# Performance work log

Measured on AMD Instinct MI355X. Metric: run time of the kernel, lower is better.

Reference implementation:

```python
import jax, jax.numpy as jnp
import numpy as np

TOPK = 13
N_CLASSES = 80
EPS = 1e-9
IOU_EPS = 1e-7


def _make_anchors():
    # YOLOv8 640x640, strides 8/16/32 -> 8400 anchor points (pixel coords, cell centers)
    pts, strides = [], []
    for s in (8, 16, 32):
        n = 640 // s
        c = (np.arange(n, dtype=np.float32) + 0.5) * s
        xs, ys = np.meshgrid(c, c)
        pts.append(np.stack([xs.ravel(), ys.ravel()], -1))
        strides.append(np.full((n * n, 1), s, np.float32))
    return np.concatenate(pts).astype(np.float32), np.concatenate(strides)


def setup_inputs() -> dict:
    key = jax.random.key(0)
    k1, k2, k3, k4, k5 = jax.random.split(key, 5)
    B, G, C = 64, 32, N_CLASSES
    anc, strd = _make_anchors()
    A = anc.shape[0]  # 8400
    # positive l,t,r,b distances so decoded pred boxes are valid
    dist = jnp.abs(jax.random.normal(k1, (B, 4, A))) * 16.0 + 1.0
    cls = jax.random.normal(k2, (B, C, A))
    preds = jnp.concatenate([dist, cls], axis=1)  # (B, 4+C, A)
    x1y1 = jax.random.uniform(k3, (B, G, 2)) * 560.0
    wh = jax.random.uniform(k4, (B, G, 2)) * 64.0 + 8.0
    gt_bboxes = jnp.concatenate([x1y1, x1y1 + wh], axis=-1)  # (B, G, 4) xyxy
    gt_classes = jax.random.randint(k5, (B, G), 0, C)
    return {"preds": preds, "gt_bboxes": gt_bboxes, "gt_classes": gt_classes,
            "anchor_points": jnp.asarray(anc), "stride_tensor": jnp.asarray(strd)}


def _iou_xyxy(a, b):
    # a: (B,A,1,4), b: (B,1,G,4) -> (B,A,G)
    lt = jnp.maximum(a[..., :2], b[..., :2])
    rb = jnp.minimum(a[..., 2:], b[..., 2:])
    wh = jnp.clip(rb - lt, 0.0)
    inter = wh[..., 0] * wh[..., 1]
    area_a = (a[..., 2] - a[..., 0]) * (a[..., 3] - a[..., 1])
    area_b = (b[..., 2] - b[..., 0]) * (b[..., 3] - b[..., 1])
    return inter / (area_a + area_b - inter + IOU_EPS)


def _assign(preds, gt_bboxes, gt_classes, anchor_points, stride_tensor):
    B, G, _ = gt_bboxes.shape
    A = anchor_points.shape[0]
    dist = jnp.transpose(preds[:, :4, :], (0, 2, 1))       # (B,A,4) l,t,r,b
    pred_cls = jnp.transpose(preds[:, 4:, :], (0, 2, 1))    # (B,A,C)
    # dist2bbox (xyxy)
    pb = jnp.concatenate([anchor_points[None] - dist[..., :2],
                          anchor_points[None] + dist[..., 2:]], axis=-1)  # (B,A,4)
    ious = _iou_xyxy(pb[:, :, None, :], gt_bboxes[:, None, :, :])          # (B,A,G)
    probs = jax.nn.softmax(pred_cls, axis=-1)                              # (B,A,C)
    idx_cls = jnp.broadcast_to(gt_classes[:, None, :], (B, A, G))
    cls_score = jnp.take_along_axis(probs, idx_cls, axis=-1)               # (B,A,G)
    align = jnp.sqrt(jnp.maximum(ious, 1e-12)) * jnp.sqrt(jnp.maximum(cls_score, 1e-12))
    # top-k over anchors (dim=1) -> scatter boolean mask
    mt = jnp.transpose(align, (0, 2, 1))                                   # (B,G,A)
    _, idx = jax.lax.top_k(mt, TOPK)                                       # (B,G,TOPK)
    bi = jnp.arange(B)[:, None, None]
    gi = jnp.arange(G)[None, :, None]
    mask = jnp.zeros((B, G, A), bool).at[bi, gi, idx].set(True)
    mask = jnp.transpose(mask, (0, 2, 1))                                  # (B,A,G)
    # anchors inside gt boxes
    d = jnp.concatenate([anchor_points[None, :, None, :] - gt_bboxes[:, None, :, :2],
                         gt_bboxes[:, None, :, 2:] - anchor_points[None, :, None, :]], axis=-1)
    mask = mask & (jnp.min(d, axis=-1) > EPS)
    # anchors assigned to multiple gts keep the highest-IoU gt
    multi = mask.sum(-1) > 1                                               # (B,A)
    best = jnp.argmax(ious, axis=-1)[..., None] == jnp.arange(G)[None, None, :]
    mask = jnp.where(multi[..., None], best, mask)
    fg = mask.any(-1)                                                      # (B,A)
    tgt_idx = jnp.argmax(mask, axis=-1)                                    # (B,A)
    tb = jnp.take_along_axis(gt_bboxes, tgt_idx[..., None], axis=1) * fg[..., None].astype(gt_bboxes.dtype)
    tc = jnp.where(fg, jnp.take_along_axis(gt_classes, tgt_idx, axis=1), 0)
    ts = jnp.take_along_axis(align, tgt_idx[..., None], axis=2)[..., 0] * fg.astype(align.dtype)
    return tb, tc, ts, fg, fg.sum()


def reference(preds, gt_bboxes, gt_classes, anchor_points, stride_tensor):
    return _assign(preds, gt_bboxes, gt_classes, anchor_points, stride_tensor)
```

## Files before the change

kernel.cpp:

```cpp
#include <hip/hip_runtime.h>
#include <cfloat>
#include <cstdint>
#include <climits>

#define NB 64
#define NG 32
#define NC 80
#define NA 8400
#define KTOP 13
#define CHUNK 256
#define NCH 33
#define NCAND (NCH * KTOP)
#define GGRP 16

#define CE(ka, ia, kb, ib)                                            \
    {                                                                 \
        const bool sw = (ka < kb) || (ka == kb && ia > ib);           \
        const unsigned tk = sw ? kb : ka;                             \
        const int      ti = sw ? ib : ia;                             \
        kb = sw ? ka : kb;  ib = sw ? ia : ib;                        \
        ka = tk;            ia = ti;                                  \
    }

__device__ __forceinline__ int wave_max_pos(int m) {
    m = max(m, __builtin_amdgcn_update_dpp(0, m, 0x111, 0xF, 0xF, true));
    m = max(m, __builtin_amdgcn_update_dpp(0, m, 0x112, 0xF, 0xF, true));
    m = max(m, __builtin_amdgcn_update_dpp(0, m, 0x114, 0xF, 0xF, true));
    m = max(m, __builtin_amdgcn_update_dpp(0, m, 0x118, 0xF, 0xF, true));
    m = max(m, __builtin_amdgcn_update_dpp(0, m, 0x142, 0xF, 0xF, true));
    m = max(m, __builtin_amdgcn_update_dpp(0, m, 0x143, 0xF, 0xF, true));
    return __builtin_amdgcn_readlane(m, 63);
}

__global__ __launch_bounds__(256, 2) void fusedAB(
    const float* __restrict__ preds,
    const float* __restrict__ gt_bboxes,
    const int*   __restrict__ gt_classes,
    const float* __restrict__ anchor_points,
    float2*      __restrict__ aux_ws,
    unsigned*    __restrict__ inside32,
    int*         __restrict__ bestg,
    float*       __restrict__ candv,
    int*         __restrict__ candi,
    float*       __restrict__ out_sum)
{
    __shared__ float sx1[NG], sy1[NG], sx2[NG], sy2[NG], sarea[NG];
    __shared__ int   scls[NG];
    __shared__ __align__(16) float salign[GGRP][CHUNK];
    __shared__ __align__(16) float sdist[4][CHUNK];

    const int tid   = threadIdx.x;
    const int chunk = blockIdx.x;
    const int b     = blockIdx.y;
    const int abase = chunk * CHUNK;
    const int a0    = abase + tid;
    const bool live = (a0 < NA);

    if (tid < NG) {
        const float* gb = gt_bboxes + ((size_t)b * NG + tid) * 4;
        const float x1 = gb[0], y1 = gb[1], x2 = gb[2], y2 = gb[3];
        sx1[tid] = x1; sy1[tid] = y1; sx2[tid] = x2; sy2[tid] = y2;
        sarea[tid] = (x2 - x1) * (y2 - y1);
        scls[tid]  = gt_classes[b * NG + tid];
    }
    if (b == 0 && chunk == 0 && tid == 0) out_sum[0] = 0.0f;

    {
        const int p = tid >> 6, k = tid & 63;
        float4 v = make_float4(0.0f, 0.0f, 0.0f, 0.0f);
        if (abase + 4 * k < NA)
            v = *(const float4*)(preds + ((size_t)b * (4 + NC) + p) * NA + abase + 4 * k);
        *(float4*)&sdist[p][4 * k] = v;
    }
    __syncthreads();

    float ax = 0, ay = 0, x1 = 0, y1 = 0, x2 = 0, y2 = 0, area = 0;
    if (live) {
        const float2 ap = *(const float2*)(anchor_points + (size_t)a0 * 2);
        ax = ap.x; ay = ap.y;
        const float l  = sdist[0][tid];
        const float t  = sdist[1][tid];
        const float r  = sdist[2][tid];
        const float bo = sdist[3][tid];
        x1 = ax - l; y1 = ay - t; x2 = ax + r; y2 = ay + bo;
        area = (x2 - x1) * (y2 - y1);
    }

    const float* cb = preds + ((size_t)b * (4 + NC) + 4) * NA + a0;

    float cls[NC];
    if (live) {
#pragma unroll
        for (int c = 0; c < NC; ++c) cls[c] = cb[(size_t)c * NA];
    } else {
#pragma unroll
        for (int c = 0; c < NC; ++c) cls[c] = 0.0f;
    }
#pragma unroll
    for (int c = 0; c < NC; ++c) asm volatile("" : "+v"(cls[c]));

    float m0 = cls[0], m1 = cls[1], m2 = cls[2], m3 = cls[3];
#pragma unroll
    for (int c = 4; c < NC; c += 4) {
        m0 = fmaxf(m0, cls[c]);
        m1 = fmaxf(m1, cls[c + 1]);
        m2 = fmaxf(m2, cls[c + 2]);
        m3 = fmaxf(m3, cls[c + 3]);
    }
    const float mx = fmaxf(fmaxf(m0, m1), fmaxf(m2, m3));

    float d = 0.0f;
#pragma unroll
    for (int c = 0; c < NC; ++c) d += __expf(cls[c] - mx);
    const float rd = 1.0f / d;

    unsigned ins = 0u;
    int   bg = 0;
    float bi = -1.0f;

    const int lane = tid & 63;
    const int wid  = tid >> 6;

    for (int grp = 0; grp < 2; ++grp) {
        if (live) {
            float cvl[GGRP];
#pragma unroll
            for (int gg = 0; gg < GGRP; ++gg)
                cvl[gg] = cb[(size_t)scls[grp * GGRP + gg] * NA];
#pragma unroll
            for (int gg = 0; gg < GGRP; ++gg) {
                const int g = grp * GGRP + gg;
                const float bx1 = sx1[g], by1 = sy1[g], bx2 = sx2[g], by2 = sy2[g];
                const float sag = sarea[g];
                const float ltx = fmaxf(x1, bx1), lty = fmaxf(y1, by1);
                const float rbx = fminf(x2, bx2), rby = fminf(y2, by2);
                const float w = fmaxf(rbx - ltx, 0.0f), h = fmaxf(rby - lty, 0.0f);
                const float inter = w * h;
                const float iou = inter / (area + sag - inter + 1e-7f);
                if (iou > bi) { bi = iou; bg = g; }
                const float cv = __expf(cvl[gg] - mx) * rd;
                const float al = sqrtf(fmaxf(iou, 1e-12f)) * sqrtf(fmaxf(cv, 1e-12f));
                const float dmin = fminf(fminf(ax - bx1, ay - by1), fminf(bx2 - ax, by2 - ay));
                if (dmin > 1e-9f) ins |= (1u << g);
                salign[gg][tid] = al;
            }
        } else {
#pragma unroll
            for (int gg = 0; gg < GGRP; ++gg) salign[gg][tid] = 0.0f;
        }
        __syncthreads();

        {
            const int gg0 = wid * 4;
            const float4 qA = *(const float4*)&salign[gg0 + 0][lane * 4];
            const float4 qB = *(const float4*)&salign[gg0 + 1][lane * 4];
            const float4 qC = *(const float4*)&salign[gg0 + 2][lane * 4];
            const float4 qD = *(const float4*)&salign[gg0 + 3][lane * 4];
            unsigned A0 = __float_as_uint(qA.x), A1 = __float_as_uint(qA.y);
            unsigned A2 = __float_as_uint(qA.z), A3 = __float_as_uint(qA.w);
            unsigned B0 = __float_as_uint(qB.x), B1 = __float_as_uint(qB.y);
            unsigned B2 = __float_as_uint(qB.z), B3 = __float_as_uint(qB.w);
            unsigned C0 = __float_as_uint(qC.x), C1 = __float_as_uint(qC.y);
            unsigned C2 = __float_as_uint(qC.z), C3 = __float_as_uint(qC.w);
            unsigned D0 = __float_as_uint(qD.x), D1 = __float_as_uint(qD.y);
            unsigned D2 = __float_as_uint(qD.z), D3 = __float_as_uint(qD.w);
            int IA0 = abase + lane * 4, IA1 = IA0 + 1, IA2 = IA0 + 2, IA3 = IA0 + 3;
            int IB0 = IA0, IB1 = IA1, IB2 = IA2, IB3 = IA3;
            int IC0 = IA0, IC1 = IA1, IC2 = IA2, IC3 = IA3;
            int ID0 = IA0, ID1 = IA1, ID2 = IA2, ID3 = IA3;

            CE(A0, IA0, A2, IA2); CE(A1, IA1, A3, IA3);
            CE(A0, IA0, A1, IA1); CE(A2, IA2, A3, IA3);
            CE(A1, IA1, A2, IA2);
            CE(B0, IB0, B2, IB2); CE(B1, IB1, B3, IB3);
            CE(B0, IB0, B1, IB1); CE(B2, IB2, B3, IB3);
            CE(B1, IB1, B2, IB2);
            CE(C0, IC0, C2, IC2); CE(C1, IC1, C3, IC3);
            CE(C0, IC0, C1, IC1); CE(C2, IC2, C3, IC3);
            CE(C1, IC1, C2, IC2);
            CE(D0, ID0, D2, ID2); CE(D1, ID1, D3, ID3);
            CE(D0, ID0, D1, ID1); CE(D2, ID2, D3, ID3);
            CE(D1, ID1, D2, ID2);

            unsigned rvA = 0u, rvB = 0u, rvC = 0u, rvD = 0u;
            int      riA = 0x7FFFFFFF, riB = 0x7FFFFFFF, riC = 0x7FFFFFFF, riD = 0x7FFFFFFF;
#pragma unroll
            for (int r = 0; r < KTOP; ++r) {
                const unsigned mA = (unsigned)wave_max_pos((int)A0);
                const unsigned mB = (unsigned)wave_max_pos((int)B0);
                const unsigned mC = (unsigned)wave_max_pos((int)C0);
                const unsigned mD = (unsigned)wave_max_pos((int)D0);
                const unsigned long long blA = __ballot(A0 == mA);
                const unsigned long long blB = __ballot(B0 == mB);
                const unsigned long long blC = __ballot(C0 == mC);
                const unsigned long long blD = __ballot(D0 == mD);
                const int wA = __ffsll(blA) - 1;
                const int wB = __ffsll(blB) - 1;
                const int wC = __ffsll(blC) - 1;
                const int wD = __ffsll(blD) - 1;
                const int xA = __builtin_amdgcn_readlane(IA0, wA);
                const int xB = __builtin_amdgcn_readlane(IB0, wB);
                const int xC = __builtin_amdgcn_readlane(IC0, wC);
                const int xD = __builtin_amdgcn_readlane(ID0, wD);
                if (lane == wA) { A0 = A1; IA0 = IA1; A1 = A2; IA1 = IA2; A2 = A3; IA2 = IA3; A3 = 0u; }
                if (lane == wB) { B0 = B1; IB0 = IB1; B1 = B2; IB1 = IB2; B2 = B3; IB2 = IB3; B3 = 0u; }
                if (lane == wC) { C0 = C1; IC0 = IC1; C1 = C2; IC1 = IC2; C2 = C3; IC2 = IC3; C3 = 0u; }
                if (lane == wD) { D0 = D1; ID0 = ID1; D1 = D2; ID1 = ID2; D2 = D3; ID2 = ID3; D3 = 0u; }
                if (lane == r) {
                    rvA = mA; riA = xA; rvB = mB; riB = xB;
                    rvC = mC; riC = xC; rvD = mD; riD = xD;
                }
            }
            if (lane < KTOP) {
                const int gbase = b * NG + grp * GGRP + gg0;
                const size_t b0 = ((size_t)(gbase + 0) * NCH + chunk) * KTOP + lane;
                const size_t b1 = ((size_t)(gbase + 1) * NCH + chunk) * KTOP + lane;
                const size_t b2 = ((size_t)(gbase + 2) * NCH + chunk) * KTOP + lane;
                const size_t b3 = ((size_t)(gbase + 3) * NCH + chunk) * KTOP + lane;
                candv[b0] = __uint_as_float(rvA);  candi[b0] = riA;
                candv[b1] = __uint_as_float(rvB);  candi[b1] = riB;
                candv[b2] = __uint_as_float(rvC);  candi[b2] = riC;
                candv[b3] = __uint_as_float(rvD);  candi[b3] = riD;
            }
        }
        __syncthreads();
    }

    if (live) {
        const int i = b * NA + a0;
        aux_ws[i] = make_float2(mx, rd);
        inside32[i] = ins;
        bestg[i]    = bg;
    }
}

__global__ __launch_bounds__(256) void mergeTopK(
    const float* __restrict__ candv,
    const int*   __restrict__ candi,
    int*         __restrict__ topk13)
{
    const int tid  = threadIdx.x;
    const int lane = tid & 63;
    const int row  = blockIdx.x * 4 + (tid >> 6);
    const size_t base = (size_t)row * NCAND;

    float v0 = -FLT_MAX, v1 = -FLT_MAX, v2 = -FLT_MAX, v3 = -FLT_MAX,
          v4 = -FLT_MAX, v5 = -FLT_MAX, v6 = -FLT_MAX;
    int   d0 = 0x7FFFFFFF, d1 = 0x7FFFFFFF, d2 = 0x7FFFFFFF, d3 = 0x7FFFFFFF,
          d4 = 0x7FFFFFFF, d5 = 0x7FFFFFFF, d6 = 0x7FFFFFFF;

#pragma unroll
    for (int k = 0; k < 7; ++k) {
        const int j0 = lane + 64 * k;
        if (j0 < NCAND) {
            const float x  = candv[base + j0];
            const int   xi = candi[base + j0];
            int r = 0;
            r += (v0 > x) || (v0 == x && d0 < xi);
            r += (v1 > x) || (v1 == x && d1 < xi);
            r += (v2 > x) || (v2 == x && d2 < xi);
            r += (v3 > x) || (v3 == x && d3 < xi);
            r += (v4 > x) || (v4 == x && d4 < xi);
            r += (v5 > x) || (v5 == x && d5 < xi);
            r += (v6 > x) || (v6 == x && d6 < xi);
            v6 = (6 < r) ? v6 : ((6 == r) ? x : v5);  d6 = (6 < r) ? d6 : ((6 == r) ? xi : d5);
            v5 = (5 < r) ? v5 : ((5 == r) ? x : v4);  d5 = (5 < r) ? d5 : ((5 == r) ? xi : d4);
            v4 = (4 < r) ? v4 : ((4 == r) ? x : v3);  d4 = (4 < r) ? d4 : ((4 == r) ? xi : d3);
            v3 = (3 < r) ? v3 : ((3 == r) ? x : v2);  d3 = (3 < r) ? d3 : ((3 == r) ? xi : d2);
            v2 = (2 < r) ? v2 : ((2 == r) ? x : v1);  d2 = (2 < r) ? d2 : ((2 == r) ? xi : d1);
            v1 = (1 < r) ? v1 : ((1 == r) ? x : v0);  d1 = (1 < r) ? d1 : ((1 == r) ? xi : d0);
            v0 = (0 == r) ? x  : v0;                  d0 = (0 == r) ? xi : d0;
        }
    }

    int ri = 0x7FFFFFFF;
#pragma unroll
    for (int rnd = 0; rnd < KTOP; ++rnd) {
        const int hk = __float_as_int(v0);
        const int mk = wave_max_pos(hk);
        const int key2 = (hk == mk) ? (INT_MAX - d0) : -1;
        const int mk2  = wave_max_pos(key2);
        const int midx = INT_MAX - mk2;
        if (hk == mk && d0 == midx) {
            v0 = v1; d0 = d1; v1 = v2; d1 = d2; v2 = v3; d2 = d3;
            v3 = v4; d3 = d4; v4 = v5; d4 = d5; v5 = v6; d5 = d6;
            v6 = -FLT_MAX; d6 = 0x7FFFFFFF;
        }
        if (lane == rnd) ri = midx;
    }
    if (lane < KTOP) topk13[(size_t)row * KTOP + lane] = ri;
}

__global__ __launch_bounds__(256) void phaseC(
    const float*    __restrict__ gt_bboxes,
    const int*      __restrict__ gt_classes,
    const float*    __restrict__ preds,
    const float*    __restrict__ anchor_points,
    const float2*   __restrict__ aux_ws,
    const int*      __restrict__ topk13,
    const unsigned* __restrict__ inside32,
    const int*      __restrict__ bestg,
    float*          __restrict__ out)
{
    __shared__ unsigned smask[CHUNK];
    __shared__ float ssum[4];

    const int tid   = threadIdx.x;
    const int b     = blockIdx.y;
    const int abase = blockIdx.x * CHUNK;
    const int a     = abase + tid;

    smask[tid] = 0u;
    __syncthreads();
    for (int j = tid; j < NG * KTOP; j += 256) {
        const int idx = topk13[(size_t)b * NG * KTOP + j];
        const int rel = idx - abase;
        if (rel >= 0 && rel < CHUNK)
            atomicOr(&smask[rel], 1u << (j / KTOP));
    }
    __syncthreads();

    bool fg = false;
    if (a < NA) {
        const int i = b * NA + a;
        unsigned m = smask[tid] & inside32[i];
        const int cnt = __popc(m);

        int tgt;
        if (cnt > 1)       { tgt = bestg[i];     fg = true;  }
        else if (cnt == 1) { tgt = __ffs(m) - 1; fg = true;  }
        else               { tgt = 0;            fg = false; }

        const float f = fg ? 1.0f : 0.0f;
        const float4 gbv = *(const float4*)(gt_bboxes + ((size_t)b * NG + tgt) * 4);
        const float gx1 = gbv.x, gy1 = gbv.y, gx2 = gbv.z, gy2 = gbv.w;
        *(float4*)(out + (size_t)i * 4) = make_float4(gx1 * f, gy1 * f, gx2 * f, gy2 * f);

        const size_t BA = (size_t)NB * NA;
        out[BA * 4 + i] = fg ? (float)gt_classes[b * NG + tgt] : 0.0f;

        float ts = 0.0f;
        if (fg) {
            const float2 ap = *(const float2*)(anchor_points + (size_t)a * 2);
            const float* db = preds + (size_t)b * (4 + NC) * NA + a;
            const float l  = db[0];
            const float t  = db[(size_t)NA];
            const float r  = db[(size_t)2 * NA];
            const float bo = db[(size_t)3 * NA];
            const float x1 = ap.x - l, y1 = ap.y - t, x2 = ap.x + r, y2 = ap.y + bo;
            const float2 ax = aux_ws[i];
            const float areaA = (x2 - x1) * (y2 - y1);
            const float sag   = (gx2 - gx1) * (gy2 - gy1);
            const float ltx = fmaxf(x1, gx1), lty = fmaxf(y1, gy1);
            const float rbx = fminf(x2, gx2), rby = fminf(y2, gy2);
            const float w = fmaxf(rbx - ltx, 0.0f), h = fmaxf(rby - lty, 0.0f);
            const float inter = w * h;
            const float iou = inter / (areaA + sag - inter + 1e-7f);
            const int cls = gt_classes[b * NG + tgt];
            const float cv = __expf(db[(size_t)(4 + cls) * NA] - ax.x) * ax.y;
            ts = sqrtf(fmaxf(iou, 1e-12f)) * sqrtf(fmaxf(cv, 1e-12f));
        }
        out[BA * 5 + i] = ts;
        out[BA * 6 + i] = f;
    }

    const unsigned long long ball = __ballot(fg);
    if ((tid & 63) == 0) ssum[tid >> 6] = (float)__popcll(ball);
    __syncthreads();
    if (tid == 0) {
        const float s = ssum[0] + ssum[1] + ssum[2] + ssum[3];
        if (s != 0.0f) atomicAdd(&out[(size_t)NB * NA * 7], s);
    }
}

extern "C" void kernel_launch(void* const* d_in, const int* in_sizes, int n_in,
                              void* d_out, int out_size, void* d_ws, size_t ws_size,
                              hipStream_t stream) {
    const float* preds         = (const float*)d_in[0];
    const float* gt_bboxes     = (const float*)d_in[1];
    const int*   gt_classes    = (const int*)  d_in[2];
    const float* anchor_points = (const float*)d_in[3];

    float* out = (float*)d_out;
    const size_t BA = (size_t)NB * NA;

    char* ws = (char*)d_ws;
    size_t off = 0;
    float2*   aux_ws   = (float2*)(ws + off);   off += BA * sizeof(float2);
    unsigned* inside32 = (unsigned*)(ws + off); off += BA * sizeof(unsigned);
    int*      bestg    = (int*)(ws + off);      off += BA * sizeof(int);
    float*    candv    = (float*)(ws + off);    off += (size_t)NB * NG * NCAND * sizeof(float);
    int*      candi    = (int*)(ws + off);      off += (size_t)NB * NG * NCAND * sizeof(int);
    int*      topk13   = (int*)(ws + off);

    fusedAB<<<dim3(NCH, NB), 256, 0, stream>>>(preds, gt_bboxes, gt_classes, anchor_points,
                                               aux_ws, inside32, bestg,
                                               candv, candi, out + BA * 7);

    mergeTopK<<<NB * NG / 4, 256, 0, stream>>>(candv, candi, topk13);

    phaseC<<<dim3(NCH, NB), 256, 0, stream>>>(gt_bboxes, gt_classes, preds, anchor_points,
                                              aux_ws, topk13,
                                              inside32, bestg, out);
}
```

Measured before the change: 332.0 us.

## Process 512 anchors per block and halve top-k candidate count

Each fusedAB block now covers 512 anchors, two per thread, and each lane sorts 8 alignment values instead of 4 before the wave-wide 13-round top-k selection. This halves the number of per-chunk selection passes and the candidate list written per gt, so mergeTopK scans 4 candidates per lane instead of 7. The cost is more registers per thread for the second anchor's class scores and IoU state, a longer sorting network, and half as many blocks, which may reduce occupancy and latency hiding.

```diff
diff --git a/kernel.cpp b/kernel.cpp
--- a/kernel.cpp
+++ b/kernel.cpp
@@ -8,9 +8,11 @@
 #define NC 80
 #define NA 8400
 #define KTOP 13
+#define CHUNKF 512
+#define NCHF 17
+#define NCAND (NCHF * KTOP)
 #define CHUNK 256
 #define NCH 33
-#define NCAND (NCH * KTOP)
 #define GGRP 16
 
 #define CE(ka, ia, kb, ib)                                            \
@@ -30,6 +32,44 @@
     m = max(m, __builtin_amdgcn_update_dpp(0, m, 0x142, 0xF, 0xF, true));
     m = max(m, __builtin_amdgcn_update_dpp(0, m, 0x143, 0xF, 0xF, true));
     return __builtin_amdgcn_readlane(m, 63);
+}
+
+struct TK {
+    unsigned k0, k1, k2, k3, k4, k5, k6, k7;
+    int      i0, i1, i2, i3, i4, i5, i6, i7;
+};
+
+__device__ __forceinline__ void sort8(TK& s) {
+    CE(s.k0, s.i0, s.k1, s.i1); CE(s.k2, s.i2, s.k3, s.i3);
+    CE(s.k4, s.i4, s.k5, s.i5); CE(s.k6, s.i6, s.k7, s.i7);
+    CE(s.k0, s.i0, s.k2, s.i2); CE(s.k1, s.i1, s.k3, s.i3);
+    CE(s.k4, s.i4, s.k6, s.i6); CE(s.k5, s.i5, s.k7, s.i7);
+    CE(s.k1, s.i1, s.k2, s.i2); CE(s.k5, s.i5, s.k6, s.i6);
+    CE(s.k0, s.i0, s.k4, s.i4); CE(s.k1, s.i1, s.k5, s.i5);
+    CE(s.k2, s.i2, s.k6, s.i6); CE(s.k3, s.i3, s.k7, s.i7);
+    CE(s.k2, s.i2, s.k4, s.i4); CE(s.k3, s.i3, s.k5, s.i5);
+    CE(s.k1, s.i1, s.k2, s.i2); CE(s.k3, s.i3, s.k4, s.i4);
+    CE(s.k5, s.i5, s.k6, s.i6);
+}
+
+__device__ __forceinline__ TK load8(const float* row, int lane, int abase) {
+    const float4 lo = *(const float4*)&row[lane * 8];
+    const float4 hi = *(const float4*)&row[lane * 8 + 4];
+    TK s;
+    s.k0 = __float_as_uint(lo.x); s.k1 = __float_as_uint(lo.y);
+    s.k2 = __float_as_uint(lo.z); s.k3 = __float_as_uint(lo.w);
+    s.k4 = __float_as_uint(hi.x); s.k5 = __float_as_uint(hi.y);
+    s.k6 = __float_as_uint(hi.z); s.k7 = __float_as_uint(hi.w);
+    s.i0 = abase + lane * 8; s.i1 = s.i0 + 1; s.i2 = s.i0 + 2; s.i3 = s.i0 + 3;
+    s.i4 = s.i0 + 4; s.i5 = s.i0 + 5; s.i6 = s.i0 + 6; s.i7 = s.i0 + 7;
+    return s;
+}
+
+__device__ __forceinline__ void pop8(TK& s) {
+    s.k0 = s.k1; s.i0 = s.i1; s.k1 = s.k2; s.i1 = s.i2;
+    s.k2 = s.k3; s.i2 = s.i3; s.k3 = s.k4; s.i3 = s.i4;
+    s.k4 = s.k5; s.i4 = s.i5; s.k5 = s.k6; s.i5 = s.i6;
+    s.k6 = s.k7; s.i6 = s.i7; s.k7 = 0u;
 }
 
 __global__ __launch_bounds__(256, 2) void fusedAB(
@@ -46,15 +86,17 @@
 {
     __shared__ float sx1[NG], sy1[NG], sx2[NG], sy2[NG], sarea[NG];
     __shared__ int   scls[NG];
-    __shared__ __align__(16) float salign[GGRP][CHUNK];
-    __shared__ __align__(16) float sdist[4][CHUNK];
+    __shared__ __align__(16) float salign[GGRP][CHUNKF];
+    __shared__ __align__(16) float sdist[4][CHUNKF];
 
     const int tid   = threadIdx.x;
     const int chunk = blockIdx.x;
     const int b     = blockIdx.y;
-    const int abase = chunk * CHUNK;
-    const int a0    = abase + tid;
-    const bool live = (a0 < NA);
+    const int abase = chunk * CHUNKF;
+    const int aA    = abase + tid;
+    const int aB    = aA + 256;
+    const bool liveA = (aA < NA);
+    const bool liveB = (aB < NA);
 
     if (tid < NG) {
         const float* gb = gt_bboxes + ((size_t)b * NG + tid) * 4;
@@ -65,8 +107,10 @@
     }
     if (b == 0 && chunk == 0 && tid == 0) out_sum[0] = 0.0f;
 
-    {
-        const int p = tid >> 6, k = tid & 63;
+#pragma unroll
+    for (int i = 0; i < 2; ++i) {
+        const int idx = tid + i * 256;
+        const int p = idx >> 7, k = idx & 127;
         float4 v = make_float4(0.0f, 0.0f, 0.0f, 0.0f);
         if (abase + 4 * k < NA)
             v = *(const float4*)(preds + ((size_t)b * (4 + NC) + p) * NA + abase + 4 * k);
@@ -74,138 +118,149 @@
     }
     __syncthreads();
 
-    float ax = 0, ay = 0, x1 = 0, y1 = 0, x2 = 0, y2 = 0, area = 0;
-    if (live) {
-        const float2 ap = *(const float2*)(anchor_points + (size_t)a0 * 2);
-        ax = ap.x; ay = ap.y;
-        const float l  = sdist[0][tid];
-        const float t  = sdist[1][tid];
-        const float r  = sdist[2][tid];
-        const float bo = sdist[3][tid];
-        x1 = ax - l; y1 = ay - t; x2 = ax + r; y2 = ay + bo;
-        area = (x2 - x1) * (y2 - y1);
-    }
-
-    const float* cb = preds + ((size_t)b * (4 + NC) + 4) * NA + a0;
-
-    float cls[NC];
-    if (live) {
-#pragma unroll
-        for (int c = 0; c < NC; ++c) cls[c] = cb[(size_t)c * NA];
+    float axA = 0, ayA = 0, x1A = 0, y1A = 0, x2A = 0, y2A = 0, areaA = 0;
+    float axB = 0, ayB = 0, x1B = 0, y1B = 0, x2B = 0, y2B = 0, areaB = 0;
+    if (liveA) {
+        const float2 ap = *(const float2*)(anchor_points + (size_t)aA * 2);
+        axA = ap.x; ayA = ap.y;
+        const float l = sdist[0][tid], t = sdist[1][tid];
+        const float r = sdist[2][tid], bo = sdist[3][tid];
+        x1A = axA - l; y1A = ayA - t; x2A = axA + r; y2A = ayA + bo;
+        areaA = (x2A - x1A) * (y2A - y1A);
+    }
+    if (liveB) {
+        const float2 ap = *(const float2*)(anchor_points + (size_t)aB * 2);
+        axB = ap.x; ayB = ap.y;
+        const float l = sdist[0][tid + 256], t = sdist[1][tid + 256];
+        const float r = sdist[2][tid + 256], bo = sdist[3][tid + 256];
+        x1B = axB - l; y1B = ayB - t; x2B = axB + r; y2B = ayB + bo;
+        areaB = (x2B - x1B) * (y2B - y1B);
+    }
+
+    const float* cbA = preds + ((size_t)b * (4 + NC) + 4) * NA + aA;
+    const float* cbB = cbA + 256;
+
+    float clsA[NC];
+    if (liveA) {
+#pragma unroll
+        for (int c = 0; c < NC; ++c) clsA[c] = cbA[(size_t)c * NA];
     } else {
 #pragma unroll
-        for (int c = 0; c < NC; ++c) cls[c] = 0.0f;
-    }
-#pragma unroll
-    for (int c = 0; c < NC; ++c) asm volatile("" : "+v"(cls[c]));
-
-    float m0 = cls[0], m1 = cls[1], m2 = cls[2], m3 = cls[3];
+        for (int c = 0; c < NC; ++c) clsA[c] = 0.0f;
+    }
+    float mA0 = clsA[0], mA1 = clsA[1], mA2 = clsA[2], mA3 = clsA[3];
 #pragma unroll
     for (int c = 4; c < NC; c += 4) {
-        m0 = fmaxf(m0, cls[c]);
-        m1 = fmaxf(m1, cls[c + 1]);
-        m2 = fmaxf(m2, cls[c + 2]);
-        m3 = fmaxf(m3, cls[c + 3]);
-    }
-    const float mx = fmaxf(fmaxf(m0, m1), fmaxf(m2, m3));
-
-    float d = 0.0f;
-#pragma unroll
-    for (int c = 0; c < NC; ++c) d += __expf(cls[c] - mx);
-    const float rd = 1.0f / d;
-
-    unsigned ins = 0u;
-    int   bg = 0;
-    float bi = -1.0f;
+        mA0 = fmaxf(mA0, clsA[c]);     mA1 = fmaxf(mA1, clsA[c + 1]);
+        mA2 = fmaxf(mA2, clsA[c + 2]); mA3 = fmaxf(mA3, clsA[c + 3]);
+    }
+    const float mxA = fmaxf(fmaxf(mA0, mA1), fmaxf(mA2, mA3));
+    float dA = 0.0f;
+#pragma unroll
+    for (int c = 0; c < NC; ++c) dA += __expf(clsA[c] - mxA);
+    const float rdA = 1.0f / dA;
+
+    float clsB[NC];
+    if (liveB) {
+#pragma unroll
+        for (int c = 0; c < NC; ++c) clsB[c] = cbB[(size_t)c * NA];
+    } else {
+#pragma unroll
+        for (int c = 0; c < NC; ++c) clsB[c] = 0.0f;
+    }
+    float mB0 = clsB[0], mB1 = clsB[1], mB2 = clsB[2], mB3 = clsB[3];
+#pragma unroll
+    for (int c = 4; c < NC; c += 4) {
+        mB0 = fmaxf(mB0, clsB[c]);     mB1 = fmaxf(mB1, clsB[c + 1]);
+        mB2 = fmaxf(mB2, clsB[c + 2]); mB3 = fmaxf(mB3, clsB[c + 3]);
+    }
+    const float mxB = fmaxf(fmaxf(mB0, mB1), fmaxf(mB2, mB3));
+    float dB = 0.0f;
+#pragma unroll
+    for (int c = 0; c < NC; ++c) dB += __expf(clsB[c] - mxB);
+    const float rdB = 1.0f / dB;
+
+    unsigned insA = 0u, insB = 0u;
+    int   bgA = 0, bgB = 0;
+    float biA = -1.0f, biB = -1.0f;
 
     const int lane = tid & 63;
     const int wid  = tid >> 6;
 
     for (int grp = 0; grp < 2; ++grp) {
-        if (live) {
-            float cvl[GGRP];
-#pragma unroll
-            for (int gg = 0; gg < GGRP; ++gg)
-                cvl[gg] = cb[(size_t)scls[grp * GGRP + gg] * NA];
-#pragma unroll
-            for (int gg = 0; gg < GGRP; ++gg) {
-                const int g = grp * GGRP + gg;
-                const float bx1 = sx1[g], by1 = sy1[g], bx2 = sx2[g], by2 = sy2[g];
-                const float sag = sarea[g];
-                const float ltx = fmaxf(x1, bx1), lty = fmaxf(y1, by1);
-                const float rbx = fminf(x2, bx2), rby = fminf(y2, by2);
+        float cvlA[GGRP], cvlB[GGRP];
+#pragma unroll
+        for (int gg = 0; gg < GGRP; ++gg) {
+            const int g = grp * GGRP + gg;
+            cvlA[gg] = liveA ? cbA[(size_t)scls[g] * NA] : 0.0f;
+            cvlB[gg] = liveB ? cbB[(size_t)scls[g] * NA] : 0.0f;
+        }
+#pragma unroll
+        for (int gg = 0; gg < GGRP; ++gg) {
+            const int g = grp * GGRP + gg;
+            const float bx1 = sx1[g], by1 = sy1[g], bx2 = sx2[g], by2 = sy2[g];
+            const float sag = sarea[g];
+            {
+                const float ltx = fmaxf(x1A, bx1), lty = fmaxf(y1A, by1);
+                const float rbx = fminf(x2A, bx2), rby = fminf(y2A, by2);
                 const float w = fmaxf(rbx - ltx, 0.0f), h = fmaxf(rby - lty, 0.0f);
                 const float inter = w * h;
-                const float iou = inter / (area + sag - inter + 1e-7f);
-                if (iou > bi) { bi = iou; bg = g; }
-                const float cv = __expf(cvl[gg] - mx) * rd;
+                const float iou = inter / (areaA + sag - inter + 1e-7f);
+                if (iou > biA) { biA = iou; bgA = g; }
+                const float cv = __expf(cvlA[gg] - mxA) * rdA;
                 const float al = sqrtf(fmaxf(iou, 1e-12f)) * sqrtf(fmaxf(cv, 1e-12f));
-                const float dmin = fminf(fminf(ax - bx1, ay - by1), fminf(bx2 - ax, by2 - ay));
-                if (dmin > 1e-9f) ins |= (1u << g);
-                salign[gg][tid] = al;
+                const float dmin = fminf(fminf(axA - bx1, ayA - by1), fminf(bx2 - axA, by2 - ayA));
+                if (dmin > 1e-9f) insA |= (1u << g);
+                salign[gg][tid] = liveA ? al : 0.0f;
             }
-        } else {
-#pragma unroll
-            for (int gg = 0; gg < GGRP; ++gg) salign[gg][tid] = 0.0f;
+            {
+                const float ltx = fmaxf(x1B, bx1), lty = fmaxf(y1B, by1);
+                const float rbx = fminf(x2B, bx2), rby = fminf(y2B, by2);
+                const float w = fmaxf(rbx - ltx, 0.0f), h = fmaxf(rby - lty, 0.0f);
+                const float inter = w * h;
+                const float iou = inter / (areaB + sag - inter + 1e-7f);
+                if (iou > biB) { biB = iou; bgB = g; }
+                const float cv = __expf(cvlB[gg] - mxB) * rdB;
+                const float al = sqrtf(fmaxf(iou, 1e-12f)) * sqrtf(fmaxf(cv, 1e-12f));
+                const float dmin = fminf(fminf(axB - bx1, ayB - by1), fminf(bx2 - axB, by2 - ayB));
+                if (dmin > 1e-9f) insB |= (1u << g);
+                salign[gg][tid + 256] = liveB ? al : 0.0f;
+            }
         }
         __syncthreads();
 
         {
             const int gg0 = wid * 4;
-            const float4 qA = *(const float4*)&salign[gg0 + 0][lane * 4];
-            const float4 qB = *(const float4*)&salign[gg0 + 1][lane * 4];
-            const float4 qC = *(const float4*)&salign[gg0 + 2][lane * 4];
-            const float4 qD = *(const float4*)&salign[gg0 + 3][lane * 4];
-            unsigned A0 = __float_as_uint(qA.x), A1 = __float_as_uint(qA.y);
-            unsigned A2 = __float_as_uint(qA.z), A3 = __float_as_uint(qA.w);
-            unsigned B0 = __float_as_uint(qB.x), B1 = __float_as_uint(qB.y);
-            unsigned B2 = __float_as_uint(qB.z), B3 = __float_as_uint(qB.w);
-            unsigned C0 = __float_as_uint(qC.x), C1 = __float_as_uint(qC.y);
-            unsigned C2 = __float_as_uint(qC.z), C3 = __float_as_uint(qC.w);
-            unsigned D0 = __float_as_uint(qD.x), D1 = __float_as_uint(qD.y);
-            unsigned D2 = __float_as_uint(qD.z), D3 = __float_as_uint(qD.w);
-            int IA0 = abase + lane * 4, IA1 = IA0 + 1, IA2 = IA0 + 2, IA3 = IA0 + 3;
-            int IB0 = IA0, IB1 = IA1, IB2 = IA2, IB3 = IA3;
-            int IC0 = IA0, IC1 = IA1, IC2 = IA2, IC3 = IA3;
-            int ID0 = IA0, ID1 = IA1, ID2 = IA2, ID3 = IA3;
-
-            CE(A0, IA0, A2, IA2); CE(A1, IA1, A3, IA3);
-            CE(A0, IA0, A1, IA1); CE(A2, IA2, A3, IA3);
-            CE(A1, IA1, A2, IA2);
-            CE(B0, IB0, B2, IB2); CE(B1, IB1, B3, IB3);
-            CE(B0, IB0, B1, IB1); CE(B2, IB2, B3, IB3);
-            CE(B1, IB1, B2, IB2);
-            CE(C0, IC0, C2, IC2); CE(C1, IC1, C3, IC3);
-            CE(C0, IC0, C1, IC1); CE(C2, IC2, C3, IC3);
-            CE(C1, IC1, C2, IC2);
-            CE(D0, ID0, D2, ID2); CE(D1, ID1, D3, ID3);
-            CE(D0, ID0, D1, ID1); CE(D2, ID2, D3, ID3);
-            CE(D1, ID1, D2, ID2);
+            TK sA = load8(&salign[gg0 + 0][0], lane, abase);
+            TK sB = load8(&salign[gg0 + 1][0], lane, abase);
+            TK sC = load8(&salign[gg0 + 2][0], lane, abase);
+            TK sD = load8(&salign[gg0 + 3][0], lane, abase);
+            sort8(sA); sort8(sB); sort8(sC); sort8(sD);
 
             unsigned rvA = 0u, rvB = 0u, rvC = 0u, rvD = 0u;
             int      riA = 0x7FFFFFFF, riB = 0x7FFFFFFF, riC = 0x7FFFFFFF, riD = 0x7FFFFFFF;
 #pragma unroll
             for (int r = 0; r < KTOP; ++r) {
-                const unsigned mA = (unsigned)wave_max_pos((int)A0);
-                const unsigned mB = (unsigned)wave_max_pos((int)B0);
-                const unsigned mC = (unsigned)wave_max_pos((int)C0);
-                const unsigned mD = (unsigned)wave_max_pos((int)D0);
-                const unsigned long long blA = __ballot(A0 == mA);
-                const unsigned long long blB = __ballot(B0 == mB);
-                const unsigned long long blC = __ballot(C0 == mC);
-                const unsigned long long blD = __ballot(D0 == mD);
+                const unsigned mA = (unsigned)wave_max_pos((int)sA.k0);
+                const unsigned mB = (unsigned)wave_max_pos((int)sB.k0);
+                const unsigned mC = (unsigned)wave_max_pos((int)sC.k0);
+                const unsigned mD = (unsigned)wave_max_pos((int)sD.k0);
+                const unsigned long long blA = __ballot(sA.k0 == mA);
+                const unsigned long long blB = __ballot(sB.k0 == mB);
+                const unsigned long long blC = __ballot(sC.k0 == mC);
+                const unsigned long long blD = __ballot(sD.k0 == mD);
                 const int wA = __ffsll(blA) - 1;
                 const int wB = __ffsll(blB) - 1;
                 const int wC = __ffsll(blC) - 1;
                 const int wD = __ffsll(blD) - 1;
-                const int xA = __builtin_amdgcn_readlane(IA0, wA);
-                const int xB = __builtin_amdgcn_readlane(IB0, wB);
-                const int xC = __builtin_amdgcn_readlane(IC0, wC);
-                const int xD = __builtin_amdgcn_readlane(ID0, wD);
-                if (lane == wA) { A0 = A1; IA0 = IA1; A1 = A2; IA1 = IA2; A2 = A3; IA2 = IA3; A3 = 0u; }
-                if (lane == wB) { B0 = B1; IB0 = IB1; B1 = B2; IB1 = IB2; B2 = B3; IB2 = IB3; B3 = 0u; }
-                if (lane == wC) { C0 = C1; IC0 = IC1; C1 = C2; IC1 = IC2; C2 = C3; IC2 = IC3; C3 = 0u; }
-                if (lane == wD) { D0 = D1; ID0 = ID1; D1 = D2; ID1 = ID2; D2 = D3; ID2 = ID3; D3 = 0u; }
+                const int xA = __builtin_amdgcn_readlane(sA.i0, wA);
+                const int xB = __builtin_amdgcn_readlane(sB.i0, wB);
+                const int xC = __builtin_amdgcn_readlane(sC.i0, wC);
+                const int xD = __builtin_amdgcn_readlane(sD.i0, wD);
+                if (lane == wA) pop8(sA);
+                if (lane == wB) pop8(sB);
+                if (lane == wC) pop8(sC);
+                if (lane == wD) pop8(sD);
                 if (lane == r) {
                     rvA = mA; riA = xA; rvB = mB; riB = xB;
                     rvC = mC; riC = xC; rvD = mD; riD = xD;
@@ -213,10 +268,10 @@
             }
             if (lane < KTOP) {
                 const int gbase = b * NG + grp * GGRP + gg0;
-                const size_t b0 = ((size_t)(gbase + 0) * NCH + chunk) * KTOP + lane;
-                const size_t b1 = ((size_t)(gbase + 1) * NCH + chunk) * KTOP + lane;
-                const size_t b2 = ((size_t)(gbase + 2) * NCH + chunk) * KTOP + lane;
-                const size_t b3 = ((size_t)(gbase + 3) * NCH + chunk) * KTOP + lane;
+                const size_t b0 = ((size_t)(gbase + 0) * NCHF + chunk) * KTOP + lane;
+                const size_t b1 = ((size_t)(gbase + 1) * NCHF + chunk) * KTOP + lane;
+                const size_t b2 = ((size_t)(gbase + 2) * NCHF + chunk) * KTOP + lane;
+                const size_t b3 = ((size_t)(gbase + 3) * NCHF + chunk) * KTOP + lane;
                 candv[b0] = __uint_as_float(rvA);  candi[b0] = riA;
                 candv[b1] = __uint_as_float(rvB);  candi[b1] = riB;
                 candv[b2] = __uint_as_float(rvC);  candi[b2] = riC;
@@ -226,11 +281,17 @@
         __syncthreads();
     }
 
-    if (live) {
-        const int i = b * NA + a0;
-        aux_ws[i] = make_float2(mx, rd);
-        inside32[i] = ins;
-        bestg[i]    = bg;
+    if (liveA) {
+        const int i = b * NA + aA;
+        aux_ws[i] = make_float2(mxA, rdA);
+        inside32[i] = insA;
+        bestg[i]    = bgA;
+    }
+    if (liveB) {
+        const int i = b * NA + aB;
+        aux_ws[i] = make_float2(mxB, rdB);
+        inside32[i] = insB;
+        bestg[i]    = bgB;
     }
 }
 
@@ -244,13 +305,11 @@
     const int row  = blockIdx.x * 4 + (tid >> 6);
     const size_t base = (size_t)row * NCAND;
 
-    float v0 = -FLT_MAX, v1 = -FLT_MAX, v2 = -FLT_MAX, v3 = -FLT_MAX,
-          v4 = -FLT_MAX, v5 = -FLT_MAX, v6 = -FLT_MAX;
-    int   d0 = 0x7FFFFFFF, d1 = 0x7FFFFFFF, d2 = 0x7FFFFFFF, d3 = 0x7FFFFFFF,
-          d4 = 0x7FFFFFFF, d5 = 0x7FFFFFFF, d6 = 0x7FFFFFFF;
-
-#pragma unroll
-    for (int k = 0; k < 7; ++k) {
+    float v0 = -FLT_MAX, v1 = -FLT_MAX, v2 = -FLT_MAX, v3 = -FLT_MAX;
+    int   d0 = 0x7FFFFFFF, d1 = 0x7FFFFFFF, d2 = 0x7FFFFFFF, d3 = 0x7FFFFFFF;
+
+#pragma unroll
+    for (int k = 0; k < 4; ++k) {
         const int j0 = lane + 64 * k;
         if (j0 < NCAND) {
             const float x  = candv[base + j0];
@@ -260,12 +319,6 @@
             r += (v1 > x) || (v1 == x && d1 < xi);
             r += (v2 > x) || (v2 == x && d2 < xi);
             r += (v3 > x) || (v3 == x && d3 < xi);
-            r += (v4 > x) || (v4 == x && d4 < xi);
-            r += (v5 > x) || (v5 == x && d5 < xi);
-            r += (v6 > x) || (v6 == x && d6 < xi);
-            v6 = (6 < r) ? v6 : ((6 == r) ? x : v5);  d6 = (6 < r) ? d6 : ((6 == r) ? xi : d5);
-            v5 = (5 < r) ? v5 : ((5 == r) ? x : v4);  d5 = (5 < r) ? d5 : ((5 == r) ? xi : d4);
-            v4 = (4 < r) ? v4 : ((4 == r) ? x : v3);  d4 = (4 < r) ? d4 : ((4 == r) ? xi : d3);
             v3 = (3 < r) ? v3 : ((3 == r) ? x : v2);  d3 = (3 < r) ? d3 : ((3 == r) ? xi : d2);
             v2 = (2 < r) ? v2 : ((2 == r) ? x : v1);  d2 = (2 < r) ? d2 : ((2 == r) ? xi : d1);
             v1 = (1 < r) ? v1 : ((1 == r) ? x : v0);  d1 = (1 < r) ? d1 : ((1 == r) ? xi : d0);
@@ -283,8 +336,7 @@
         const int midx = INT_MAX - mk2;
         if (hk == mk && d0 == midx) {
             v0 = v1; d0 = d1; v1 = v2; d1 = d2; v2 = v3; d2 = d3;
-            v3 = v4; d3 = d4; v4 = v5; d4 = d5; v5 = v6; d5 = d6;
-            v6 = -FLT_MAX; d6 = 0x7FFFFFFF;
+            v3 = -FLT_MAX; d3 = 0x7FFFFFFF;
         }
         if (lane == rnd) ri = midx;
     }
@@ -393,9 +445,9 @@
     int*      candi    = (int*)(ws + off);      off += (size_t)NB * NG * NCAND * sizeof(int);
     int*      topk13   = (int*)(ws + off);
 
-    fusedAB<<<dim3(NCH, NB), 256, 0, stream>>>(preds, gt_bboxes, gt_classes, anchor_points,
-                                               aux_ws, inside32, bestg,
-                                               candv, candi, out + BA * 7);
+    fusedAB<<<dim3(NCHF, NB), 256, 0, stream>>>(preds, gt_bboxes, gt_classes, anchor_points,
+                                                aux_ws, inside32, bestg,
+                                                candv, candi, out + BA * 7);
 
     mergeTopK<<<NB * NG / 4, 256, 0, stream>>>(candv, candi, topk13);
 
```

New measurement: 366.0 us. 1.1x slower.
